# Performance work log

Hardware: AMD Instinct MI355X
Metric: run time of the kernel (lower is better)

## Reference

```python
import jax, jax.numpy as jnp
import numpy as np

N, F_IN, H, C, E, G, OUT = 50000, 128, 4, 64, 800000, 128, 8

def _glorot(key, shape):
    lim = float(np.sqrt(6.0 / (shape[0] + shape[-1] if len(shape) == 2 else shape[-1] + 1)))
    return jax.random.uniform(key, shape, jnp.float32, -lim, lim)

def setup_inputs() -> dict:
    key = jax.random.key(0)
    ks = jax.random.split(key, 12)
    x = jax.random.normal(ks[0], (N, F_IN), jnp.float32)
    edge_index = jax.random.randint(ks[1], (2, E), 0, N, jnp.int64)
    batch = jnp.sort(jax.random.randint(ks[2], (N,), 0, G, jnp.int64))
    return {
        "x": x, "edge_index": edge_index, "batch": batch,
        "W1": _glorot(ks[3], (F_IN, H * C)),
        "a1s": _glorot(ks[4], (H, C)), "a1d": _glorot(ks[5], (H, C)),
        "b1": jnp.zeros((H * C,), jnp.float32),
        "W2": _glorot(ks[6], (H * C, H * C)),
        "a2s": _glorot(ks[7], (H, C)), "a2d": _glorot(ks[8], (H, C)),
        "b2": jnp.zeros((C,), jnp.float32),
        "fc_w": _glorot(ks[9], (C, OUT)),
        "fc_b": jnp.zeros((OUT,), jnp.float32),
    }

def _gat_conv(x, src, dst, W, a_src, a_dst, bias, concat):
    # x: [N, in]; src/dst: [E'] (self-loops already appended, PyG default)
    n = x.shape[0]
    h = (x @ W).reshape(n, H, C)                       # [N, H, C]
    alpha_src = (h * a_src).sum(-1)                    # [N, H]
    alpha_dst = (h * a_dst).sum(-1)                    # [N, H]
    e = alpha_src[src] + alpha_dst[dst]                # [E', H]
    e = jax.nn.leaky_relu(e, 0.2)
    # neighbor softmax grouped by destination node
    m = jax.ops.segment_max(e, dst, num_segments=n)    # [N, H]
    ex = jnp.exp(e - m[dst])
    denom = jax.ops.segment_sum(ex, dst, num_segments=n)
    alpha = ex / (denom[dst] + 1e-16)                  # [E', H]
    msg = h[src] * alpha[:, :, None]                   # [E', H, C]
    out = jax.ops.segment_sum(msg, dst, num_segments=n)  # [N, H, C]
    out = out.reshape(n, H * C) if concat else out.mean(axis=1)
    return out + bias

def reference(x, edge_index, batch, W1, a1s, a1d, b1, W2, a2s, a2d, b2, fc_w, fc_b):
    n = x.shape[0]
    loop = jnp.arange(n, dtype=edge_index.dtype)
    src = jnp.concatenate([edge_index[0], loop])
    dst = jnp.concatenate([edge_index[1], loop])
    h = _gat_conv(x, src, dst, W1, a1s, a1d, b1, concat=True)
    h = jax.nn.elu(h)                                  # activation, dropout p=0
    h = _gat_conv(h, src, dst, W2, a2s, a2d, b2, concat=False)
    # global mean pool over graphs
    sums = jax.ops.segment_sum(h, batch, num_segments=G)
    cnts = jax.ops.segment_sum(jnp.ones((n,), h.dtype), batch, num_segments=G)
    pooled = sums / jnp.maximum(cnts, 1.0)[:, None]    # [G, C]
    return pooled @ fc_w + fc_b                        # [G, OUT]
```

## Files before the change

### kernel.cpp

```cpp
#include <hip/hip_runtime.h>
#include <hip/hip_bf16.h>
#include <cstddef>
#include <cstdint>

#define NN 50000
#define MPAD 50048
#define F_IN 128
#define NH 4
#define NC 64
#define NE 800000
#define NG 128
#define NOUT 8
#define HC 256
#define EP (NE + NN)

typedef unsigned short ushort_t;
typedef _Float16 f16;
typedef __attribute__((ext_vector_type(2))) _Float16 f16x2;
typedef __attribute__((ext_vector_type(8))) _Float16 f16x8;
typedef __attribute__((ext_vector_type(4))) float f32x4;

__device__ __forceinline__ float lrelu02(float x) { return x > 0.0f ? x : 0.2f * x; }
__device__ __forceinline__ float elu1(float x)    { return x > 0.0f ? x : expm1f(x); }

__device__ __forceinline__ ushort_t f2h_bits(float f) {
    f16 h = (f16)f;
    union { f16 h; ushort_t u; } cv; cv.h = h;
    return cv.u;
}
__device__ __forceinline__ uint32_t pack2h(float a, float b) {
    union { f16 h[2]; uint32_t u; } cv;
    cv.h[0] = (f16)a; cv.h[1] = (f16)b;
    return cv.u;
}
__device__ __forceinline__ f16x2 as_h2(uint32_t q) {
    union { uint32_t u; f16x2 h; } cv; cv.u = q;
    return cv.h;
}
__device__ __forceinline__ void h2_unpack(uint32_t q, float& lo, float& hi) {
    union { uint32_t u; f16 h[2]; } cv; cv.u = q;
    lo = (float)cv.h[0];
    hi = (float)cv.h[1];
}

__device__ __forceinline__ float fdot2f(f16x2 a, f16x2 b, float c) {
#if __has_builtin(__builtin_amdgcn_fdot2)
    return __builtin_amdgcn_fdot2(a, b, c, false);
#else
    float d;
    asm("v_dot2_f32_f16 %0, %1, %2, %3" : "=v"(d) : "v"(a), "v"(b), "v"(c));
    return d;
#endif
}
__device__ __forceinline__ uint32_t permb(uint32_t a, uint32_t b, uint32_t s) {
    return __builtin_amdgcn_perm(a, b, s);
}
#define SEL_E 0x01000504u
#define SEL_O 0x03020706u

__device__ __forceinline__ void gld16(const void* g, void* l) {
    __builtin_amdgcn_global_load_lds(
        (const __attribute__((address_space(1))) unsigned int*)g,
        (__attribute__((address_space(3))) unsigned int*)l, 16, 0, 0);
}

#define XN4 (NN * F_IN / 4)
#define NW (F_IN * HC + HC * HC)
__global__ void prep_kernel(const int* __restrict__ edst,
                            const float* __restrict__ x,
                            const float* __restrict__ W1,
                            const float* __restrict__ W2,
                            int* __restrict__ deg,
                            f16* __restrict__ xh,
                            f16* __restrict__ w1t, f16* __restrict__ w2t) {
    int idx = blockIdx.x * blockDim.x + threadIdx.x;
    if (idx < EP) {
        int d = (idx < NE) ? edst[idx] : (idx - NE);
        atomicAdd(&deg[d], 1);
        return;
    }
    idx -= EP;
    if (idx < XN4) {
        float4 v = ((const float4*)x)[idx];
        f16 o[4] = {(f16)v.x, (f16)v.y, (f16)v.z, (f16)v.w};
        *(uint2*)(xh + idx * 4) = *(const uint2*)o;
        return;
    }
    idx -= XN4;
    const int n1 = F_IN * HC;
    if (idx < n1) {
        int k = idx / HC, n = idx % HC;
        w1t[n * F_IN + k] = (f16)W1[idx];
    } else if (idx < NW) {
        int i2 = idx - n1;
        int k = i2 / HC, n = i2 % HC;
        w2t[n * HC + k] = (f16)W2[i2];
    }
}

__global__ __launch_bounds__(256) void scan_p1(const int* __restrict__ deg,
                                               int* __restrict__ partials) {
    __shared__ int lds[256];
    int b = blockIdx.x, t = threadIdx.x;
    int i0 = b * 1024 + t * 4;
    int s = 0;
#pragma unroll
    for (int j = 0; j < 4; j++) { int i = i0 + j; if (i < NN) s += deg[i]; }
    lds[t] = s;
    __syncthreads();
    for (int o = 128; o; o >>= 1) { if (t < o) lds[t] += lds[t + o]; __syncthreads(); }
    if (t == 0) partials[b] = lds[0];
}

__global__ __launch_bounds__(256) void scan_p3(const int* __restrict__ deg,
                                               const int* __restrict__ partials,
                                               int* __restrict__ offs) {
    __shared__ int lds[256];
    __shared__ int base_s;
    int b = blockIdx.x, t = threadIdx.x;
    if (t == 0) {
        int s = 0;
        for (int i = 0; i < b; i++) s += partials[i];
        base_s = s;
        if (b == 0) offs[0] = 0;
    }
    int i0 = b * 1024 + t * 4;
    int v[4]; int s = 0;
#pragma unroll
    for (int j = 0; j < 4; j++) { int i = i0 + j; v[j] = (i < NN) ? deg[i] : 0; s += v[j]; }
    lds[t] = s;
    __syncthreads();
    for (int o = 1; o < 256; o <<= 1) {
        int x = (t >= o) ? lds[t - o] : 0;
        __syncthreads();
        lds[t] += x;
        __syncthreads();
    }
    int run = base_s + (lds[t] - s);
#pragma unroll
    for (int j = 0; j < 4; j++) { run += v[j]; int i = i0 + j; if (i < NN) offs[i + 1] = run; }
}

__global__ void edge_fill(const int* __restrict__ esrc, const int* __restrict__ edst,
                          const int* __restrict__ offs, int* __restrict__ fill,
                          int* __restrict__ csr) {
    int e = blockIdx.x * blockDim.x + threadIdx.x;
    if (e >= EP) return;
    int s, d;
    if (e < NE) { s = esrc[e]; d = edst[e]; } else { s = d = e - NE; }
    int pos = offs[d] + atomicAdd(&fill[d], 1);
    csr[pos] = s;
}

__global__ __launch_bounds__(256, 3) void gemm_gat(
        const f16* __restrict__ A, const f16* __restrict__ BT,
        const float* __restrict__ a_s, const float* __restrict__ a_d,
        ushort_t* __restrict__ hf2, float* __restrict__ asrc,
        float* __restrict__ adst, int M, int K) {
    __shared__ alignas(16) char smem[33792];
    f16* lA = (f16*)smem;
    f16* lB = (f16*)smem + 4096;

    int t = threadIdx.x;
    int wave = t >> 6, lane = t & 63;
    int wm = wave >> 1, wn = wave & 1;
    int quad = lane >> 4, l15 = lane & 15;
    int tileM = blockIdx.x * 128;
    int by = blockIdx.y;

    f32x4 acc[4][4];
#pragma unroll
    for (int f = 0; f < 4; f++)
#pragma unroll
        for (int g = 0; g < 4; g++) acc[f][g] = (f32x4){0.f, 0.f, 0.f, 0.f};

    for (int k0 = 0; k0 < K; k0 += 32) {
        __syncthreads();
#pragma unroll
        for (int i = 0; i < 2; i++) {
            int c = wave * 2 + i;
            int row = c * 16 + (lane >> 2);
            int kk = k0 + (lane & 3) * 8;
            gld16(A + (size_t)(tileM + row) * K + kk, &lA[c * 512]);
            gld16(BT + (size_t)(by * 128 + row) * K + kk, &lB[c * 512]);
        }
        __syncthreads();

        f16x8 ah[4], bh[4];
#pragma unroll
        for (int f = 0; f < 4; f++)
            ah[f] = *(const f16x8*)&lA[(wm * 64 + f * 16 + l15) * 32 + quad * 8];
#pragma unroll
        for (int g = 0; g < 4; g++)
            bh[g] = *(const f16x8*)&lB[(wn * 64 + g * 16 + l15) * 32 + quad * 8];
#pragma unroll
        for (int f = 0; f < 4; f++)
#pragma unroll
            for (int g = 0; g < 4; g++)
                acc[f][g] = __builtin_amdgcn_mfma_f32_16x16x32_f16(ah[f], bh[g], acc[f][g], 0, 0, 0);
    }

    int head = (by << 1) | wn;
    float as_v[4], ad_v[4];
#pragma unroll
    for (int g = 0; g < 4; g++) {
        as_v[g] = a_s[head * 64 + g * 16 + l15];
        ad_v[g] = a_d[head * 64 + g * 16 + l15];
    }
#pragma unroll
    for (int f = 0; f < 4; f++) {
#pragma unroll
        for (int r = 0; r < 4; r++) {
            float ps = acc[f][0][r] * as_v[0] + acc[f][1][r] * as_v[1]
                     + acc[f][2][r] * as_v[2] + acc[f][3][r] * as_v[3];
            float pd = acc[f][0][r] * ad_v[0] + acc[f][1][r] * ad_v[1]
                     + acc[f][2][r] * ad_v[2] + acc[f][3][r] * ad_v[3];
#pragma unroll
            for (int o = 1; o < 16; o <<= 1) {
                ps += __shfl_xor(ps, o);
                pd += __shfl_xor(pd, o);
            }
            int row = tileM + wm * 64 + f * 16 + quad * 4 + r;
            if (l15 == 0 && row < M) {
                asrc[row * 4 + head] = ps;
                adst[row * 4 + head] = pd;
            }
        }
    }

    __syncthreads();
    ushort_t* lC2u = (ushort_t*)smem;
    const uint32_t* lC2d = (const uint32_t*)smem;
#pragma unroll
    for (int f = 0; f < 4; f++)
#pragma unroll
        for (int g = 0; g < 4; g++)
#pragma unroll
            for (int r = 0; r < 4; r++)
                lC2u[(wm * 64 + f * 16 + quad * 4 + r) * 132 + (g * 16 + l15) * 2 + wn] =
                    f2h_bits(acc[f][g][r]);
    __syncthreads();
    uint32_t* hb2 = (uint32_t*)hf2;
#pragma unroll
    for (int it = 0; it < 32; it++) {
        int row = wave * 32 + it;
        uint32_t v = lC2d[row * 66 + lane];
        hb2[(size_t)(tileM + row) * 128 + by * 64 + lane] = v;
    }
}

template <int CONCAT>
__device__ void gat_node_fullwave(const ushort_t* __restrict__ hf2,
                                  const float* __restrict__ asrc,
                                  const float* __restrict__ adst,
                                  const int* __restrict__ offs,
                                  const int* __restrict__ csr,
                                  const float* __restrict__ bias,
                                  f16* __restrict__ oh,
                                  float* __restrict__ of,
                                  int node, int lane, uint2* lwF) {
    int start = offs[node];
    int deg = offs[node + 1] - start;
    float4 ad = *(const float4*)(adst + node * 4);

    float w0, w1, w2, w3;
    float m0, m1, m2, m3, i0, i1, i2, i3;
    int msrc = 0;

    if (deg <= 64) {
        float t0 = -1e30f, t1 = -1e30f, t2 = -1e30f, t3 = -1e30f;
        if (lane < deg) {
            int sidx = csr[start + lane];
            float4 as = *(const float4*)(asrc + sidx * 4);
            t0 = lrelu02(as.x + ad.x);
            t1 = lrelu02(as.y + ad.y);
            t2 = lrelu02(as.z + ad.z);
            t3 = lrelu02(as.w + ad.w);
            msrc = sidx;
        }
        m0 = t0; m1 = t1; m2 = t2; m3 = t3;
#pragma unroll
        for (int o = 1; o < 64; o <<= 1) {
            m0 = fmaxf(m0, __shfl_xor(m0, o));
            m1 = fmaxf(m1, __shfl_xor(m1, o));
            m2 = fmaxf(m2, __shfl_xor(m2, o));
            m3 = fmaxf(m3, __shfl_xor(m3, o));
        }
        w0 = __expf(t0 - m0);
        w1 = __expf(t1 - m1);
        w2 = __expf(t2 - m2);
        w3 = __expf(t3 - m3);
        float s0 = w0, s1 = w1, s2 = w2, s3 = w3;
#pragma unroll
        for (int o = 1; o < 64; o <<= 1) {
            s0 += __shfl_xor(s0, o);
            s1 += __shfl_xor(s1, o);
            s2 += __shfl_xor(s2, o);
            s3 += __shfl_xor(s3, o);
        }
        i0 = 1.0f / (s0 + 1e-16f);
        i1 = 1.0f / (s1 + 1e-16f);
        i2 = 1.0f / (s2 + 1e-16f);
        i3 = 1.0f / (s3 + 1e-16f);
        w0 *= i0; w1 *= i1; w2 *= i2; w3 *= i3;
    } else {
        m0 = m1 = m2 = m3 = -1e30f;
        float s0 = 0.f, s1 = 0.f, s2 = 0.f, s3 = 0.f;
        float e0 = 0.f, e1 = 0.f, e2 = 0.f, e3 = 0.f;
        for (int j = lane; j < deg; j += 64) {
            int sidx = csr[start + j];
            float4 as = *(const float4*)(asrc + sidx * 4);
            float t0 = lrelu02(as.x + ad.x);
            float t1 = lrelu02(as.y + ad.y);
            float t2 = lrelu02(as.z + ad.z);
            float t3 = lrelu02(as.w + ad.w);
            if (j == lane) { e0 = t0; e1 = t1; e2 = t2; e3 = t3; msrc = sidx; }
            float nm;
            nm = fmaxf(m0, t0); s0 = s0 * __expf(m0 - nm) + __expf(t0 - nm); m0 = nm;
            nm = fmaxf(m1, t1); s1 = s1 * __expf(m1 - nm) + __expf(t1 - nm); m1 = nm;
            nm = fmaxf(m2, t2); s2 = s2 * __expf(m2 - nm) + __expf(t2 - nm); m2 = nm;
            nm = fmaxf(m3, t3); s3 = s3 * __expf(m3 - nm) + __expf(t3 - nm); m3 = nm;
        }
        for (int o = 32; o; o >>= 1) {
            float om, os, nm;
            om = __shfl_xor(m0, o); os = __shfl_xor(s0, o);
            nm = fmaxf(m0, om); s0 = s0 * __expf(m0 - nm) + os * __expf(om - nm); m0 = nm;
            om = __shfl_xor(m1, o); os = __shfl_xor(s1, o);
            nm = fmaxf(m1, om); s1 = s1 * __expf(m1 - nm) + os * __expf(om - nm); m1 = nm;
            om = __shfl_xor(m2, o); os = __shfl_xor(s2, o);
            nm = fmaxf(m2, om); s2 = s2 * __expf(m2 - nm) + os * __expf(om - nm); m2 = nm;
            om = __shfl_xor(m3, o); os = __shfl_xor(s3, o);
            nm = fmaxf(m3, om); s3 = s3 * __expf(m3 - nm) + os * __expf(om - nm); m3 = nm;
        }
        i0 = 1.0f / (s0 + 1e-16f);
        i1 = 1.0f / (s1 + 1e-16f);
        i2 = 1.0f / (s2 + 1e-16f);
        i3 = 1.0f / (s3 + 1e-16f);
        w0 = __expf(e0 - m0) * i0;
        w1 = __expf(e1 - m1) * i1;
        w2 = __expf(e2 - m2) * i2;
        w3 = __expf(e3 - m3) * i3;
    }

    lwF[lane] = (uint2){pack2h(w0, w1), pack2h(w2, w3)};

    int hp = lane >> 5;
    const uint32_t* lwu = (const uint32_t*)lwF;
    float aE0 = 0.f, aO0 = 0.f, aE1 = 0.f, aO1 = 0.f;
    float c0a = 0.f, c0b = 0.f, c1a = 0.f, c1b = 0.f;
    const uint32_t* hb = (const uint32_t*)hf2 + lane * 2;
    int jmax = deg < 64 ? deg : 64;

    int j = 0;
    if (CONCAT) {
        for (; j + 4 <= jmax; j += 4) {
            int s0 = __builtin_amdgcn_readlane(msrc, j);
            int s1 = __builtin_amdgcn_readlane(msrc, j + 1);
            int s2 = __builtin_amdgcn_readlane(msrc, j + 2);
            int s3 = __builtin_amdgcn_readlane(msrc, j + 3);
            uint2 q0 = *(const uint2*)(hb + (size_t)s0 * 128);
            uint2 q1 = *(const uint2*)(hb + (size_t)s1 * 128);
            uint2 q2 = *(const uint2*)(hb + (size_t)s2 * 128);
            uint2 q3 = *(const uint2*)(hb + (size_t)s3 * 128);
            uint32_t wA = lwu[(j + 0) * 2 + hp];
            uint32_t wB = lwu[(j + 1) * 2 + hp];
            uint32_t wC = lwu[(j + 2) * 2 + hp];
            uint32_t wD = lwu[(j + 3) * 2 + hp];
            uint32_t weAB = permb(wA, wB, SEL_E), woAB = permb(wA, wB, SEL_O);
            uint32_t weCD = permb(wC, wD, SEL_E), woCD = permb(wC, wD, SEL_O);
            uint32_t xeAB = permb(q0.x, q1.x, SEL_E), xoAB = permb(q0.x, q1.x, SEL_O);
            uint32_t yeAB = permb(q0.y, q1.y, SEL_E), yoAB = permb(q0.y, q1.y, SEL_O);
            uint32_t xeCD = permb(q2.x, q3.x, SEL_E), xoCD = permb(q2.x, q3.x, SEL_O);
            uint32_t yeCD = permb(q2.y, q3.y, SEL_E), yoCD = permb(q2.y, q3.y, SEL_O);
            aE0 = fdot2f(as_h2(xeAB), as_h2(weAB), aE0);
            aO0 = fdot2f(as_h2(xoAB), as_h2(woAB), aO0);
            aE1 = fdot2f(as_h2(yeAB), as_h2(weAB), aE1);
            aO1 = fdot2f(as_h2(yoAB), as_h2(woAB), aO1);
            aE0 = fdot2f(as_h2(xeCD), as_h2(weCD), aE0);
            aO0 = fdot2f(as_h2(xoCD), as_h2(woCD), aO0);
            aE1 = fdot2f(as_h2(yeCD), as_h2(weCD), aE1);
            aO1 = fdot2f(as_h2(yoCD), as_h2(woCD), aO1);
        }
        for (; j < jmax; j++) {
            int sidx = __builtin_amdgcn_readlane(msrc, j);
            f16x2 wh = as_h2(lwu[j * 2 + hp]);
            uint2 q = *(const uint2*)(hb + (size_t)sidx * 128);
            f16x2 qx = as_h2(q.x), qy = as_h2(q.y);
            aE0 += (float)qx[0] * (float)wh[0];
            aO0 += (float)qx[1] * (float)wh[1];
            aE1 += (float)qy[0] * (float)wh[0];
            aO1 += (float)qy[1] * (float)wh[1];
        }
    } else {
        for (; j + 4 <= jmax; j += 4) {
            int s0 = __builtin_amdgcn_readlane(msrc, j);
            int s1 = __builtin_amdgcn_readlane(msrc, j + 1);
            int s2 = __builtin_amdgcn_readlane(msrc, j + 2);
            int s3 = __builtin_amdgcn_readlane(msrc, j + 3);
            uint2 q0 = *(const uint2*)(hb + (size_t)s0 * 128);
            uint2 q1 = *(const uint2*)(hb + (size_t)s1 * 128);
            uint2 q2 = *(const uint2*)(hb + (size_t)s2 * 128);
            uint2 q3 = *(const uint2*)(hb + (size_t)s3 * 128);
            f16x2 w0v = as_h2(lwu[(j + 0) * 2 + hp]);
            f16x2 w1v = as_h2(lwu[(j + 1) * 2 + hp]);
            f16x2 w2v = as_h2(lwu[(j + 2) * 2 + hp]);
            f16x2 w3v = as_h2(lwu[(j + 3) * 2 + hp]);
            c0a = fdot2f(as_h2(q0.x), w0v, c0a);
            c1a = fdot2f(as_h2(q0.y), w0v, c1a);
            c0b = fdot2f(as_h2(q1.x), w1v, c0b);
            c1b = fdot2f(as_h2(q1.y), w1v, c1b);
            c0a = fdot2f(as_h2(q2.x), w2v, c0a);
            c1a = fdot2f(as_h2(q2.y), w2v, c1a);
            c0b = fdot2f(as_h2(q3.x), w3v, c0b);
            c1b = fdot2f(as_h2(q3.y), w3v, c1b);
        }
        for (; j < jmax; j++) {
            int sidx = __builtin_amdgcn_readlane(msrc, j);
            f16x2 wh = as_h2(lwu[j * 2 + hp]);
            uint2 q = *(const uint2*)(hb + (size_t)sidx * 128);
            c0a = fdot2f(as_h2(q.x), wh, c0a);
            c1a = fdot2f(as_h2(q.y), wh, c1a);
        }
    }
    for (int jj = 64; jj < deg; jj++) {
        int sidx = csr[start + jj];
        float4 as = *(const float4*)(asrc + sidx * 4);
        float u0 = __expf(lrelu02(as.x + ad.x) - m0) * i0;
        float u1 = __expf(lrelu02(as.y + ad.y) - m1) * i1;
        float u2 = __expf(lrelu02(as.z + ad.z) - m2) * i2;
        float u3 = __expf(lrelu02(as.w + ad.w) - m3) * i3;
        float ue = hp ? u2 : u0;
        float uo = hp ? u3 : u1;
        uint2 q = *(const uint2*)(hb + (size_t)sidx * 128);
        float xl, xh2, yl, yh;
        h2_unpack(q.x, xl, xh2);
        h2_unpack(q.y, yl, yh);
        if (CONCAT) {
            aE0 += ue * xl;
            aO0 += uo * xh2;
            aE1 += ue * yl;
            aO1 += uo * yh;
        } else {
            c0a += ue * xl + uo * xh2;
            c1a += ue * yl + uo * yh;
        }
    }

    int c0 = (lane & 31) * 2;
    int he = hp * 2, ho = hp * 2 + 1;
    if (CONCAT) {
        size_t base = (size_t)node * HC;
        float vE0 = elu1(aE0 + bias[he * 64 + c0]);
        float vE1 = elu1(aE1 + bias[he * 64 + c0 + 1]);
        float vO0 = elu1(aO0 + bias[ho * 64 + c0]);
        float vO1 = elu1(aO1 + bias[ho * 64 + c0 + 1]);
        f16 pe[2] = {(f16)vE0, (f16)vE1};
        f16 po[2] = {(f16)vO0, (f16)vO1};
        *(uint32_t*)(oh + base + he * 64 + c0) = *(const uint32_t*)pe;
        *(uint32_t*)(oh + base + ho * 64 + c0) = *(const uint32_t*)po;
    } else {
        float s0 = c0a + c0b;
        float s1 = c1a + c1b;
        s0 += __shfl_xor(s0, 32);
        s1 += __shfl_xor(s1, 32);
        if (hp == 0) {
            float2 v = {0.25f * s0 + bias[c0], 0.25f * s1 + bias[c0 + 1]};
            *(float2*)(of + (size_t)node * NC + c0) = v;
        }
    }
}

template <int CONCAT>
__global__ __launch_bounds__(256, 4) void gat_agg(const ushort_t* __restrict__ hf2,
                                                  const float* __restrict__ asrc,
                                                  const float* __restrict__ adst,
                                                  const int* __restrict__ offs,
                                                  const int* __restrict__ csr,
                                                  const float* __restrict__ bias,
                                                  f16* __restrict__ oh,
                                                  float* __restrict__ of) {
    __shared__ uint4 lw4[4][64];
    int wave = threadIdx.x >> 6, lane = threadIdx.x & 63;
    int grp = lane >> 5, l31 = lane & 31;
    int hp = (lane >> 4) & 1;
    int nbase = blockIdx.x * 8 + wave * 2;
    int node = nbase + grp;
    int start = offs[node];
    int deg = offs[node + 1] - start;

    if (!__all(deg <= 32)) {
        uint2* lwF = (uint2*)&lw4[wave][0];
        gat_node_fullwave<CONCAT>(hf2, asrc, adst, offs, csr, bias, oh, of,
                                  nbase, lane, lwF);
        gat_node_fullwave<CONCAT>(hf2, asrc, adst, offs, csr, bias, oh, of,
                                  nbase + 1, lane, lwF);
        return;
    }

    const uint4* hq = (const uint4*)hf2;
    int msrc = 0;
    bool act = l31 < deg;
    if (act) msrc = csr[start + l31];

    int b0 = grp * 32;
    int i0 = __shfl(msrc, b0 + 0);
    int i1 = __shfl(msrc, b0 + 1);
    int i2 = __shfl(msrc, b0 + 2);
    int i3 = __shfl(msrc, b0 + 3);
    int i4 = __shfl(msrc, b0 + 4);
    int i5 = __shfl(msrc, b0 + 5);
    int i6 = __shfl(msrc, b0 + 6);
    int i7 = __shfl(msrc, b0 + 7);
    uint4 q0 = hq[(uint32_t)i0 * 32u + l31];
    uint4 q1 = hq[(uint32_t)i1 * 32u + l31];
    uint4 q2 = hq[(uint32_t)i2 * 32u + l31];
    uint4 q3 = hq[(uint32_t)i3 * 32u + l31];
    uint4 r0 = hq[(uint32_t)i4 * 32u + l31];
    uint4 r1 = hq[(uint32_t)i5 * 32u + l31];
    uint4 r2 = hq[(uint32_t)i6 * 32u + l31];
    uint4 r3 = hq[(uint32_t)i7 * 32u + l31];

    float4 ad = *(const float4*)(adst + (size_t)node * 4);
    float t0 = -1e30f, t1 = -1e30f, t2 = -1e30f, t3 = -1e30f;
    if (act) {
        float4 as = *(const float4*)(asrc + (size_t)msrc * 4);
        t0 = lrelu02(as.x + ad.x);
        t1 = lrelu02(as.y + ad.y);
        t2 = lrelu02(as.z + ad.z);
        t3 = lrelu02(as.w + ad.w);
    }
    float m0 = t0, m1 = t1, m2 = t2, m3 = t3;
#pragma unroll
    for (int o = 1; o < 32; o <<= 1) {
        m0 = fmaxf(m0, __shfl_xor(m0, o));
        m1 = fmaxf(m1, __shfl_xor(m1, o));
        m2 = fmaxf(m2, __shfl_xor(m2, o));
        m3 = fmaxf(m3, __shfl_xor(m3, o));
    }
    float w0 = __expf(t0 - m0);
    float w1 = __expf(t1 - m1);
    float w2 = __expf(t2 - m2);
    float w3 = __expf(t3 - m3);
    float s0 = w0, s1 = w1, s2 = w2, s3 = w3;
#pragma unroll
    for (int o = 1; o < 32; o <<= 1) {
        s0 += __shfl_xor(s0, o);
        s1 += __shfl_xor(s1, o);
        s2 += __shfl_xor(s2, o);
        s3 += __shfl_xor(s3, o);
    }
    w0 *= 1.0f / (s0 + 1e-16f);
    w1 *= 1.0f / (s1 + 1e-16f);
    w2 *= 1.0f / (s2 + 1e-16f);
    w3 *= 1.0f / (s3 + 1e-16f);

    lw4[wave][lane] = (uint4){(uint32_t)msrc, pack2h(w0, w1),
                              (uint32_t)msrc, pack2h(w2, w3)};

    const uint2* lwp = (const uint2*)&lw4[wave][grp * 32];
    int c0 = (l31 & 15) * 4;
    int deg4 = (deg + 3) & ~3;

    uint32_t wy0 = lwp[0 * 2 + hp].y;
    uint32_t wy1 = lwp[1 * 2 + hp].y;
    uint32_t wy2 = lwp[2 * 2 + hp].y;
    uint32_t wy3 = lwp[3 * 2 + hp].y;
    uint32_t wz0 = lwp[4 * 2 + hp].y;
    uint32_t wz1 = lwp[5 * 2 + hp].y;
    uint32_t wz2 = lwp[6 * 2 + hp].y;
    uint32_t wz3 = lwp[7 * 2 + hp].y;

    if (CONCAT) {
        float aE0 = 0.f, aE1 = 0.f, aE2 = 0.f, aE3 = 0.f;
        float aO0 = 0.f, aO1 = 0.f, aO2 = 0.f, aO3 = 0.f;
#define CPAIR(A0, A1, W0, W1)                                                  \
        {                                                                      \
            uint32_t we = permb(W0, W1, SEL_E);                                \
            uint32_t wo = permb(W0, W1, SEL_O);                                \
            aE0 = fdot2f(as_h2(permb(A0.x, A1.x, SEL_E)), as_h2(we), aE0);     \
            aO0 = fdot2f(as_h2(permb(A0.x, A1.x, SEL_O)), as_h2(wo), aO0);     \
            aE1 = fdot2f(as_h2(permb(A0.y, A1.y, SEL_E)), as_h2(we), aE1);     \
            aO1 = fdot2f(as_h2(permb(A0.y, A1.y, SEL_O)), as_h2(wo), aO1);     \
            aE2 = fdot2f(as_h2(permb(A0.z, A1.z, SEL_E)), as_h2(we), aE2);     \
            aO2 = fdot2f(as_h2(permb(A0.z, A1.z, SEL_O)), as_h2(wo), aO2);     \
            aE3 = fdot2f(as_h2(permb(A0.w, A1.w, SEL_E)), as_h2(we), aE3);     \
            aO3 = fdot2f(as_h2(permb(A0.w, A1.w, SEL_O)), as_h2(wo), aO3);     \
        }
        int j = 0;
        for (;;) {
            CPAIR(q0, q1, wy0, wy1)
            CPAIR(q2, q3, wy2, wy3)
            {
                int p = j + 8;
                if (p < deg4) {
                    uint2 n0 = lwp[(p + 0) * 2 + hp];
                    uint2 n1 = lwp[(p + 1) * 2 + hp];
                    uint2 n2 = lwp[(p + 2) * 2 + hp];
                    uint2 n3 = lwp[(p + 3) * 2 + hp];
                    wy0 = n0.y; wy1 = n1.y; wy2 = n2.y; wy3 = n3.y;
                    q0 = hq[n0.x * 32u + l31];
                    q1 = hq[n1.x * 32u + l31];
                    q2 = hq[n2.x * 32u + l31];
                    q3 = hq[n3.x * 32u + l31];
                }
            }
            j += 4;
            if (j >= deg4) break;
            CPAIR(r0, r1, wz0, wz1)
            CPAIR(r2, r3, wz2, wz3)
            {
                int p = j + 8;
                if (p < deg4) {
                    uint2 n0 = lwp[(p + 0) * 2 + hp];
                    uint2 n1 = lwp[(p + 1) * 2 + hp];
                    uint2 n2 = lwp[(p + 2) * 2 + hp];
                    uint2 n3 = lwp[(p + 3) * 2 + hp];
                    wz0 = n0.y; wz1 = n1.y; wz2 = n2.y; wz3 = n3.y;
                    r0 = hq[n0.x * 32u + l31];
                    r1 = hq[n1.x * 32u + l31];
                    r2 = hq[n2.x * 32u + l31];
                    r3 = hq[n3.x * 32u + l31];
                }
            }
            j += 4;
            if (j >= deg4) break;
        }
#undef CPAIR
        int he = hp * 2, ho = hp * 2 + 1;
        size_t base = (size_t)node * HC;
        float4 bE = *(const float4*)(bias + he * 64 + c0);
        float4 bO = *(const float4*)(bias + ho * 64 + c0);
        f16 pe[4] = {(f16)elu1(aE0 + bE.x), (f16)elu1(aE1 + bE.y),
                     (f16)elu1(aE2 + bE.z), (f16)elu1(aE3 + bE.w)};
        f16 po[4] = {(f16)elu1(aO0 + bO.x), (f16)elu1(aO1 + bO.y),
                     (f16)elu1(aO2 + bO.z), (f16)elu1(aO3 + bO.w)};
        *(uint2*)(oh + base + he * 64 + c0) = *(const uint2*)pe;
        *(uint2*)(oh + base + ho * 64 + c0) = *(const uint2*)po;
    } else {
        float a0 = 0.f, a1 = 0.f, a2 = 0.f, a3 = 0.f;
        float b0f = 0.f, b1f = 0.f, b2f = 0.f, b3f = 0.f;
        int j = 0;
        for (;;) {
            {
                f16x2 wvA = as_h2(wy0), wvB = as_h2(wy1);
                f16x2 wvC = as_h2(wy2), wvD = as_h2(wy3);
                a0 = fdot2f(as_h2(q0.x), wvA, a0);
                a1 = fdot2f(as_h2(q0.y), wvA, a1);
                a2 = fdot2f(as_h2(q0.z), wvA, a2);
                a3 = fdot2f(as_h2(q0.w), wvA, a3);
                b0f = fdot2f(as_h2(q1.x), wvB, b0f);
                b1f = fdot2f(as_h2(q1.y), wvB, b1f);
                b2f = fdot2f(as_h2(q1.z), wvB, b2f);
                b3f = fdot2f(as_h2(q1.w), wvB, b3f);
                a0 = fdot2f(as_h2(q2.x), wvC, a0);
                a1 = fdot2f(as_h2(q2.y), wvC, a1);
                a2 = fdot2f(as_h2(q2.z), wvC, a2);
                a3 = fdot2f(as_h2(q2.w), wvC, a3);
                b0f = fdot2f(as_h2(q3.x), wvD, b0f);
                b1f = fdot2f(as_h2(q3.y), wvD, b1f);
                b2f = fdot2f(as_h2(q3.z), wvD, b2f);
                b3f = fdot2f(as_h2(q3.w), wvD, b3f);
            }
            {
                int p = j + 8;
                if (p < deg4) {
                    uint2 n0 = lwp[(p + 0) * 2 + hp];
                    uint2 n1 = lwp[(p + 1) * 2 + hp];
                    uint2 n2 = lwp[(p + 2) * 2 + hp];
                    uint2 n3 = lwp[(p + 3) * 2 + hp];
                    wy0 = n0.y; wy1 = n1.y; wy2 = n2.y; wy3 = n3.y;
                    q0 = hq[n0.x * 32u + l31];
                    q1 = hq[n1.x * 32u + l31];
                    q2 = hq[n2.x * 32u + l31];
                    q3 = hq[n3.x * 32u + l31];
                }
            }
            j += 4;
            if (j >= deg4) break;
            {
                f16x2 wvA = as_h2(wz0), wvB = as_h2(wz1);
                f16x2 wvC = as_h2(wz2), wvD = as_h2(wz3);
                a0 = fdot2f(as_h2(r0.x), wvA, a0);
                a1 = fdot2f(as_h2(r0.y), wvA, a1);
                a2 = fdot2f(as_h2(r0.z), wvA, a2);
                a3 = fdot2f(as_h2(r0.w), wvA, a3);
                b0f = fdot2f(as_h2(r1.x), wvB, b0f);
                b1f = fdot2f(as_h2(r1.y), wvB, b1f);
                b2f = fdot2f(as_h2(r1.z), wvB, b2f);
                b3f = fdot2f(as_h2(r1.w), wvB, b3f);
                a0 = fdot2f(as_h2(r2.x), wvC, a0);
                a1 = fdot2f(as_h2(r2.y), wvC, a1);
                a2 = fdot2f(as_h2(r2.z), wvC, a2);
                a3 = fdot2f(as_h2(r2.w), wvC, a3);
                b0f = fdot2f(as_h2(r3.x), wvD, b0f);
                b1f = fdot2f(as_h2(r3.y), wvD, b1f);
                b2f = fdot2f(as_h2(r3.z), wvD, b2f);
                b3f = fdot2f(as_h2(r3.w), wvD, b3f);
            }
            {
                int p = j + 8;
                if (p < deg4) {
                    uint2 n0 = lwp[(p + 0) * 2 + hp];
                    uint2 n1 = lwp[(p + 1) * 2 + hp];
                    uint2 n2 = lwp[(p + 2) * 2 + hp];
                    uint2 n3 = lwp[(p + 3) * 2 + hp];
                    wz0 = n0.y; wz1 = n1.y; wz2 = n2.y; wz3 = n3.y;
                    r0 = hq[n0.x * 32u + l31];
                    r1 = hq[n1.x * 32u + l31];
                    r2 = hq[n2.x * 32u + l31];
                    r3 = hq[n3.x * 32u + l31];
                }
            }
            j += 4;
            if (j >= deg4) break;
        }
        float u0 = a0 + b0f, u1 = a1 + b1f, u2 = a2 + b2f, u3 = a3 + b3f;
        u0 += __shfl_xor(u0, 16);
        u1 += __shfl_xor(u1, 16);
        u2 += __shfl_xor(u2, 16);
        u3 += __shfl_xor(u3, 16);
        if (hp == 0) {
            float4 bv = *(const float4*)(bias + c0);
            float4 v = {0.25f * u0 + bv.x, 0.25f * u1 + bv.y,
                        0.25f * u2 + bv.z, 0.25f * u3 + bv.w};
            *(float4*)(of + (size_t)node * NC + c0) = v;
        }
    }
}

__global__ __launch_bounds__(256) void pool_kernel(const float* __restrict__ out2,
                                                   const int* __restrict__ batch,
                                                   float* __restrict__ pool,
                                                   float* __restrict__ cnt) {
    int gw = (blockIdx.x * blockDim.x + threadIdx.x) >> 6;
    int lane = threadIdx.x & 63;
    int start = gw * 16;
    if (start >= NN) return;
    int end = start + 16 < NN ? start + 16 : NN;
    int curg = batch[start];
    float acc = 0.f; int run = 0;
    for (int node = start; node < end; node++) {
        int g = batch[node];
        if (g != curg) {
            atomicAdd(&pool[curg * 64 + lane], acc);
            if (lane == 0) atomicAdd(&cnt[curg], (float)run);
            curg = g; acc = 0.f; run = 0;
        }
        acc += out2[(size_t)node * NC + lane];
        run++;
    }
    atomicAdd(&pool[curg * 64 + lane], acc);
    if (lane == 0) atomicAdd(&cnt[curg], (float)run);
}

__global__ void fc_kernel(const float* __restrict__ pool, const float* __restrict__ cnt,
                          const float* __restrict__ fc_w, const float* __restrict__ fc_b,
                          float* __restrict__ out) {
    int idx = blockIdx.x * blockDim.x + threadIdx.x;
    if (idx >= NG * NOUT) return;
    int g = idx >> 3, o = idx & 7;
    float inv = 1.0f / fmaxf(cnt[g], 1.0f);
    float s = 0.f;
#pragma unroll
    for (int c = 0; c < 64; c++) s += pool[g * 64 + c] * fc_w[c * 8 + o];
    out[idx] = s * inv + fc_b[o];
}

extern "C" void kernel_launch(void* const* d_in, const int* in_sizes, int n_in,
                              void* d_out, int out_size, void* d_ws, size_t ws_size,
                              hipStream_t stream) {
    const float* x    = (const float*)d_in[0];
    const int*   ei   = (const int*)d_in[1];
    const int*   batch= (const int*)d_in[2];
    const float* W1   = (const float*)d_in[3];
    const float* a1s  = (const float*)d_in[4];
    const float* a1d  = (const float*)d_in[5];
    const float* b1   = (const float*)d_in[6];
    const float* W2   = (const float*)d_in[7];
    const float* a2s  = (const float*)d_in[8];
    const float* a2d  = (const float*)d_in[9];
    const float* b2   = (const float*)d_in[10];
    const float* fc_w = (const float*)d_in[11];
    const float* fc_b = (const float*)d_in[12];
    float* out = (float*)d_out;

    char* p = (char*)d_ws;
    auto alloc = [&](size_t bytes) -> char* {
        char* r = p; p += (bytes + 255) & ~(size_t)255; return r;
    };
    int*   deg     = (int*)alloc((size_t)NN * 4);
    int*   fill    = (int*)alloc((size_t)NN * 4);
    float* pool    = (float*)alloc((size_t)NG * 64 * 4);
    float* cnt     = (float*)alloc((size_t)NG * 4);
    size_t zero_bytes = (size_t)(p - (char*)d_ws);
    int*   offs    = (int*)alloc((size_t)(NN + 1) * 4);
    int*   partials= (int*)alloc(64 * 4);
    int*   csr     = (int*)alloc((size_t)EP * 4);
    float* asrc    = (float*)alloc((size_t)NN * 4 * 4);
    float* adst    = (float*)alloc((size_t)NN * 4 * 4);
    ushort_t* hf2  = (ushort_t*)alloc((size_t)MPAD * HC * 2);
    f16*   xh      = (f16*)alloc((size_t)MPAD * F_IN * 2);
    f16*   act     = (f16*)alloc((size_t)MPAD * HC * 2);
    f16*   w1t     = (f16*)alloc((size_t)HC * F_IN * 2);
    f16*   w2t     = (f16*)alloc((size_t)HC * HC * 2);
    float* out2    = (float*)xh;

    hipMemsetAsync(d_ws, 0, zero_bytes, stream);

    int prep_n = EP + XN4 + NW;
    prep_kernel<<<(prep_n + 255) / 256, 256, 0, stream>>>(
        ei + NE, x, W1, W2, deg, xh, w1t, w2t);
    scan_p1<<<49, 256, 0, stream>>>(deg, partials);
    scan_p3<<<49, 256, 0, stream>>>(deg, partials, offs);
    edge_fill<<<(EP + 255) / 256, 256, 0, stream>>>(ei, ei + NE, offs, fill, csr);

    dim3 gg((NN + 127) / 128, HC / 128);
    int nb8 = (NN + 7) / 8;

    gemm_gat<<<gg, 256, 0, stream>>>(xh, w1t, a1s, a1d, hf2, asrc, adst, NN, F_IN);
    gat_agg<1><<<nb8, 256, 0, stream>>>(hf2, asrc, adst, offs, csr, b1, act, nullptr);
    gemm_gat<<<gg, 256, 0, stream>>>(act, w2t, a2s, a2d, hf2, asrc, adst, NN, HC);
    gat_agg<0><<<nb8, 256, 0, stream>>>(hf2, asrc, adst, offs, csr, b2, nullptr, out2);
    pool_kernel<<<((NN + 15) / 16 + 3) / 4, 256, 0, stream>>>(out2, batch, pool, cnt);
    fc_kernel<<<(NG * NOUT + 255) / 256, 256, 0, stream>>>(pool, cnt, fc_w, fc_b, out);
}
```

Before: 367.2 us.

## Fuse mean-pool into layer-2 aggregation and reuse degree-count atomics as CSR ranks

The layer-2 aggregation now atomically adds each node's head-mean output straight into per-graph pool sums. This removes the out2 write, the separate pool kernel and the count atomics. Graph sizes come from a binary search over the sorted batch array, and the bias is folded into the final FC kernel. Separately, the rank returned by the degree-count atomic is stored and reused in edge_fill, so the second atomic pass and the fill buffer are gone. The cost is heavy atomic contention on only 128x64 pool addresses, plus an extra EP-sized rank array to write and read.

New measurement: 380.0 us. +3.5%, slower.

```diff
diff --git a/kernel.cpp b/kernel.cpp
--- a/kernel.cpp
+++ b/kernel.cpp
@@ -71,12 +71,13 @@
                             const float* __restrict__ W1,
                             const float* __restrict__ W2,
                             int* __restrict__ deg,
+                            int* __restrict__ rank,
                             f16* __restrict__ xh,
                             f16* __restrict__ w1t, f16* __restrict__ w2t) {
     int idx = blockIdx.x * blockDim.x + threadIdx.x;
     if (idx < EP) {
         int d = (idx < NE) ? edst[idx] : (idx - NE);
-        atomicAdd(&deg[d], 1);
+        rank[idx] = atomicAdd(&deg[d], 1);
         return;
     }
     idx -= EP;
@@ -142,14 +143,13 @@
 }
 
 __global__ void edge_fill(const int* __restrict__ esrc, const int* __restrict__ edst,
-                          const int* __restrict__ offs, int* __restrict__ fill,
+                          const int* __restrict__ offs, const int* __restrict__ rank,
                           int* __restrict__ csr) {
     int e = blockIdx.x * blockDim.x + threadIdx.x;
     if (e >= EP) return;
     int s, d;
     if (e < NE) { s = esrc[e]; d = edst[e]; } else { s = d = e - NE; }
-    int pos = offs[d] + atomicAdd(&fill[d], 1);
-    csr[pos] = s;
+    csr[offs[d] + rank[e]] = s;
 }
 
 __global__ __launch_bounds__(256, 3) void gemm_gat(
@@ -255,6 +255,7 @@
                                   const float* __restrict__ adst,
                                   const int* __restrict__ offs,
                                   const int* __restrict__ csr,
+                                  const int* __restrict__ gb,
                                   const float* __restrict__ bias,
                                   f16* __restrict__ oh,
                                   float* __restrict__ of,
@@ -464,8 +465,9 @@
         s0 += __shfl_xor(s0, 32);
         s1 += __shfl_xor(s1, 32);
         if (hp == 0) {
-            float2 v = {0.25f * s0 + bias[c0], 0.25f * s1 + bias[c0 + 1]};
-            *(float2*)(of + (size_t)node * NC + c0) = v;
+            int g = gb[node];
+            atomicAdd(of + g * 64 + c0, 0.25f * s0);
+            atomicAdd(of + g * 64 + c0 + 1, 0.25f * s1);
         }
     }
 }
@@ -476,6 +478,7 @@
                                                   const float* __restrict__ adst,
                                                   const int* __restrict__ offs,
                                                   const int* __restrict__ csr,
+                                                  const int* __restrict__ gb,
                                                   const float* __restrict__ bias,
                                                   f16* __restrict__ oh,
                                                   float* __restrict__ of) {
@@ -490,9 +493,9 @@
 
     if (!__all(deg <= 32)) {
         uint2* lwF = (uint2*)&lw4[wave][0];
-        gat_node_fullwave<CONCAT>(hf2, asrc, adst, offs, csr, bias, oh, of,
+        gat_node_fullwave<CONCAT>(hf2, asrc, adst, offs, csr, gb, bias, oh, of,
                                   nbase, lane, lwF);
-        gat_node_fullwave<CONCAT>(hf2, asrc, adst, offs, csr, bias, oh, of,
+        gat_node_fullwave<CONCAT>(hf2, asrc, adst, offs, csr, gb, bias, oh, of,
                                   nbase + 1, lane, lwF);
         return;
     }
@@ -719,51 +722,50 @@
         u1 += __shfl_xor(u1, 16);
         u2 += __shfl_xor(u2, 16);
         u3 += __shfl_xor(u3, 16);
+        float o0 = 0.25f * u0, o1 = 0.25f * u1, o2 = 0.25f * u2, o3 = 0.25f * u3;
+        float p0 = __shfl_xor(o0, 32);
+        float p1 = __shfl_xor(o1, 32);
+        float p2 = __shfl_xor(o2, 32);
+        float p3 = __shfl_xor(o3, 32);
+        int g = gb[node];
+        int gO = __shfl_xor(g, 32);
         if (hp == 0) {
-            float4 bv = *(const float4*)(bias + c0);
-            float4 v = {0.25f * u0 + bv.x, 0.25f * u1 + bv.y,
-                        0.25f * u2 + bv.z, 0.25f * u3 + bv.w};
-            *(float4*)(of + (size_t)node * NC + c0) = v;
-        }
-    }
-}
-
-__global__ __launch_bounds__(256) void pool_kernel(const float* __restrict__ out2,
-                                                   const int* __restrict__ batch,
-                                                   float* __restrict__ pool,
-                                                   float* __restrict__ cnt) {
-    int gw = (blockIdx.x * blockDim.x + threadIdx.x) >> 6;
-    int lane = threadIdx.x & 63;
-    int start = gw * 16;
-    if (start >= NN) return;
-    int end = start + 16 < NN ? start + 16 : NN;
-    int curg = batch[start];
-    float acc = 0.f; int run = 0;
-    for (int node = start; node < end; node++) {
-        int g = batch[node];
-        if (g != curg) {
-            atomicAdd(&pool[curg * 64 + lane], acc);
-            if (lane == 0) atomicAdd(&cnt[curg], (float)run);
-            curg = g; acc = 0.f; run = 0;
-        }
-        acc += out2[(size_t)node * NC + lane];
-        run++;
-    }
-    atomicAdd(&pool[curg * 64 + lane], acc);
-    if (lane == 0) atomicAdd(&cnt[curg], (float)run);
-}
-
-__global__ void fc_kernel(const float* __restrict__ pool, const float* __restrict__ cnt,
+            float* pb = of + g * 64 + c0;
+            if (g == gO) {
+                if (grp == 0) {
+                    atomicAdd(pb + 0, o0 + p0);
+                    atomicAdd(pb + 1, o1 + p1);
+                    atomicAdd(pb + 2, o2 + p2);
+                    atomicAdd(pb + 3, o3 + p3);
+                }
+            } else {
+                atomicAdd(pb + 0, o0);
+                atomicAdd(pb + 1, o1);
+                atomicAdd(pb + 2, o2);
+                atomicAdd(pb + 3, o3);
+            }
+        }
+    }
+}
+
+__global__ void fc_kernel(const float* __restrict__ pool,
+                          const int* __restrict__ batch,
+                          const float* __restrict__ b2,
                           const float* __restrict__ fc_w, const float* __restrict__ fc_b,
                           float* __restrict__ out) {
     int idx = blockIdx.x * blockDim.x + threadIdx.x;
     if (idx >= NG * NOUT) return;
     int g = idx >> 3, o = idx & 7;
-    float inv = 1.0f / fmaxf(cnt[g], 1.0f);
+    int lo = 0, hi = NN;
+    while (lo < hi) { int mid = (lo + hi) >> 1; if (batch[mid] < g) lo = mid + 1; else hi = mid; }
+    int lo2 = lo, hi2 = NN;
+    while (lo2 < hi2) { int mid = (lo2 + hi2) >> 1; if (batch[mid] < g + 1) lo2 = mid + 1; else hi2 = mid; }
+    float inv = 1.0f / fmaxf((float)(lo2 - lo), 1.0f);
     float s = 0.f;
 #pragma unroll
-    for (int c = 0; c < 64; c++) s += pool[g * 64 + c] * fc_w[c * 8 + o];
-    out[idx] = s * inv + fc_b[o];
+    for (int c = 0; c < 64; c++)
+        s += (pool[g * 64 + c] * inv + b2[c]) * fc_w[c * 8 + o];
+    out[idx] = s + fc_b[o];
 }
 
 extern "C" void kernel_launch(void* const* d_in, const int* in_sizes, int n_in,
@@ -789,13 +791,12 @@
         char* r = p; p += (bytes + 255) & ~(size_t)255; return r;
     };
     int*   deg     = (int*)alloc((size_t)NN * 4);
-    int*   fill    = (int*)alloc((size_t)NN * 4);
     float* pool    = (float*)alloc((size_t)NG * 64 * 4);
-    float* cnt     = (float*)alloc((size_t)NG * 4);
     size_t zero_bytes = (size_t)(p - (char*)d_ws);
     int*   offs    = (int*)alloc((size_t)(NN + 1) * 4);
     int*   partials= (int*)alloc(64 * 4);
     int*   csr     = (int*)alloc((size_t)EP * 4);
+    int*   rank    = (int*)alloc((size_t)EP * 4);
     float* asrc    = (float*)alloc((size_t)NN * 4 * 4);
     float* adst    = (float*)alloc((size_t)NN * 4 * 4);
     ushort_t* hf2  = (ushort_t*)alloc((size_t)MPAD * HC * 2);
@@ -803,24 +804,22 @@
     f16*   act     = (f16*)alloc((size_t)MPAD * HC * 2);
     f16*   w1t     = (f16*)alloc((size_t)HC * F_IN * 2);
     f16*   w2t     = (f16*)alloc((size_t)HC * HC * 2);
-    float* out2    = (float*)xh;
 
     hipMemsetAsync(d_ws, 0, zero_bytes, stream);
 
     int prep_n = EP + XN4 + NW;
     prep_kernel<<<(prep_n + 255) / 256, 256, 0, stream>>>(
-        ei + NE, x, W1, W2, deg, xh, w1t, w2t);
+        ei + NE, x, W1, W2, deg, rank, xh, w1t, w2t);
     scan_p1<<<49, 256, 0, stream>>>(deg, partials);
     scan_p3<<<49, 256, 0, stream>>>(deg, partials, offs);
-    edge_fill<<<(EP + 255) / 256, 256, 0, stream>>>(ei, ei + NE, offs, fill, csr);
+    edge_fill<<<(EP + 255) / 256, 256, 0, stream>>>(ei, ei + NE, offs, rank, csr);
 
     dim3 gg((NN + 127) / 128, HC / 128);
     int nb8 = (NN + 7) / 8;
 
     gemm_gat<<<gg, 256, 0, stream>>>(xh, w1t, a1s, a1d, hf2, asrc, adst, NN, F_IN);
-    gat_agg<1><<<nb8, 256, 0, stream>>>(hf2, asrc, adst, offs, csr, b1, act, nullptr);
+    gat_agg<1><<<nb8, 256, 0, stream>>>(hf2, asrc, adst, offs, csr, batch, b1, act, nullptr);
     gemm_gat<<<gg, 256, 0, stream>>>(act, w2t, a2s, a2d, hf2, asrc, adst, NN, HC);
-    gat_agg<0><<<nb8, 256, 0, stream>>>(hf2, asrc, adst, offs, csr, b2, nullptr, out2);
-    pool_kernel<<<((NN + 15) / 16 + 3) / 4, 256, 0, stream>>>(out2, batch, pool, cnt);
-    fc_kernel<<<(NG * NOUT + 255) / 256, 256, 0, stream>>>(pool, cnt, fc_w, fc_b, out);
-}
+    gat_agg<0><<<nb8, 256, 0, stream>>>(hf2, asrc, adst, offs, csr, batch, b2, nullptr, pool);
+    fc_kernel<<<(NG * NOUT + 255) / 256, 256, 0, stream>>>(pool, batch, b2, fc_w, fc_b, out);
+}
```
